# Kernel optimization log

Measured on AMD Instinct MI355X. Metric: run time of the kernel, lower is better.

The kernel has to match this reference:

```python
import jax, jax.numpy as jnp
import numpy as np

B, N, D, S, H, ITERS = 8, 2048, 256, 8, 256, 3
EPS = 1e-8
LN_EPS = 1e-5
SCALE = D ** -0.5


def _ln(x):
    # normalize over last axis (affine applied separately per slot)
    mu = jnp.mean(x, axis=-1, keepdims=True)
    var = jnp.var(x, axis=-1, keepdims=True)
    return (x - mu) / jnp.sqrt(var + LN_EPS)


def setup_inputs() -> dict:
    key = jax.random.key(0)
    ks = jax.random.split(key, 24)
    w = lambda k, shape, fan_in: jax.random.normal(k, shape, jnp.float32) / np.sqrt(fan_in)
    inp = {
        "inputs": jax.random.normal(ks[0], (B, N, D), jnp.float32),
        "slot_noise": jax.random.normal(ks[1], (B, S, D), jnp.float32),
        "slots_mu": jax.random.normal(ks[2], (1, S, D), jnp.float32),
        "slots_logsigma": 0.01 * jax.random.normal(ks[3], (1, S, D), jnp.float32),
        # per-slot LayerNorm affines [S, D]
        "g_in": jnp.ones((S, D), jnp.float32), "b_in": jnp.zeros((S, D), jnp.float32),
        "g_ns": jnp.ones((S, D), jnp.float32), "b_ns": jnp.zeros((S, D), jnp.float32),
        "g_pf": jnp.ones((S, D), jnp.float32), "b_pf": jnp.zeros((S, D), jnp.float32),
        # per-slot Linear weights [S, out, in] (torch convention)
        "Wq": w(ks[4], (S, D, D), D), "bq": jnp.zeros((S, D), jnp.float32),
        "Wk": w(ks[5], (S, D, D), D), "bk": jnp.zeros((S, D), jnp.float32),
        "Wv": w(ks[6], (S, D, D), D), "bv": jnp.zeros((S, D), jnp.float32),
        # per-slot GRUCell: [S, 3D, D] (gates order r, z, n as in torch)
        "W_ih": w(ks[7], (S, 3 * D, D), D), "b_ih": jnp.zeros((S, 3 * D), jnp.float32),
        "W_hh": w(ks[8], (S, 3 * D, D), D), "b_hh": jnp.zeros((S, 3 * D), jnp.float32),
        # per-slot MLP (dim -> hidden -> dim)
        "W1": w(ks[9], (S, H, D), D), "b1": jnp.zeros((S, H), jnp.float32),
        "W2": w(ks[10], (S, D, H), H), "b2": jnp.zeros((S, D), jnp.float32),
    }
    return inp


def slot_attention_fwd(inputs, slot_noise, slots_mu, slots_logsigma,
                       g_in, b_in, g_ns, b_ns, g_pf, b_pf,
                       Wq, bq, Wk, bk, Wv, bv,
                       W_ih, b_ih, W_hh, b_hh,
                       W1, b1, W2, b2):
    # slots init: mu + sigma * noise  -> [B, S, D]
    slots = slots_mu + jnp.exp(slots_logsigma) * slot_noise

    # per-slot LayerNorm of inputs: normalization is slot-independent, affine is per-slot
    xn = _ln(inputs)  # [B, N, D]
    inputs_n = xn[:, None, :, :] * g_in[None, :, None, :] + b_in[None, :, None, :]  # [B,S,N,D]

    # per-slot k/v projections as one batched GEMM over the slot axis
    k = jnp.einsum('bsnd,sod->bsno', inputs_n, Wk) + bk[None, :, None, :]  # [B,S,N,D]
    v = jnp.einsum('bsnd,sod->bsno', inputs_n, Wv) + bv[None, :, None, :]

    attn_ori = None
    for _ in range(ITERS):
        slots_prev = slots
        sn = _ln(slots) * g_ns[None] + b_ns[None]                     # [B,S,D]
        q = jnp.einsum('bsd,sod->bso', sn, Wq) + bq[None]             # [B,S,D]
        dots = jnp.einsum('bsd,bsnd->bsn', q, k) * SCALE              # [B,S,N]
        attn_ori = jax.nn.softmax(dots, axis=1) + EPS                 # softmax over slots
        attn = attn_ori / jnp.sum(attn_ori, axis=-1, keepdims=True)   # renormalize over n
        updates = jnp.einsum('bsnd,bsn->bsd', v, attn)                # [B,S,D]

        # per-slot GRUCell: h' = (1-z)*n + z*h
        gi = jnp.einsum('bsd,sod->bso', updates, W_ih) + b_ih[None]   # [B,S,3D]
        gh = jnp.einsum('bsd,sod->bso', slots_prev, W_hh) + b_hh[None]
        gi_r, gi_z, gi_n = jnp.split(gi, 3, axis=-1)
        gh_r, gh_z, gh_n = jnp.split(gh, 3, axis=-1)
        r = jax.nn.sigmoid(gi_r + gh_r)
        z = jax.nn.sigmoid(gi_z + gh_z)
        nn_ = jnp.tanh(gi_n + r * gh_n)
        slots = (1.0 - z) * nn_ + z * slots_prev

        # per-slot MLP residual
        pre = _ln(slots) * g_pf[None] + b_pf[None]
        h1 = jax.nn.relu(jnp.einsum('bsd,shd->bsh', pre, W1) + b1[None])
        slots = slots + jnp.einsum('bsh,sdh->bsd', h1, W2) + b2[None]

    return slots, attn_ori


def reference(inputs, slot_noise, slots_mu, slots_logsigma,
              g_in, b_in, g_ns, b_ns, g_pf, b_pf,
              Wq, bq, Wk, bk, Wv, bv,
              W_ih, b_ih, W_hh, b_hh,
              W1, b1, W2, b2):
    return slot_attention_fwd(inputs, slot_noise, slots_mu, slots_logsigma,
                              g_in, b_in, g_ns, b_ns, g_pf, b_pf,
                              Wq, bq, Wk, bk, Wv, bv,
                              W_ih, b_ih, W_hh, b_hh,
                              W1, b1, W2, b2)
```

## Files before the change

### kernel.cpp

```cpp
#include <hip/hip_runtime.h>


#define BB 8
#define NT 2048
#define DD 256
#define SS 8
#define HH 256

static constexpr float F_EPS   = 1e-8f;
static constexpr float F_LNEPS = 1e-5f;
static constexpr float F_SCALE = 0.0625f;

__device__ __forceinline__ float wredsum(float v) {
#pragma unroll
  for (int m = 32; m > 0; m >>= 1) v += __shfl_xor(v, m, 64);
  return v;
}
__device__ __forceinline__ float sigm(float x) { return 1.f / (1.f + __expf(-x)); }
__device__ __forceinline__ float tanhfast(float x) {
  float ax = fabsf(x);
  float e = __expf(2.f * ax);
  float t2 = 1.f - 2.f / (e + 1.f);
  return x < 0.f ? -t2 : t2;
}
__device__ __forceinline__ int x2i(int bb, int dd) { return bb*288 + (dd>>5)*36 + (dd&31); }
__device__ __forceinline__ int xpi(int d) { return (d>>5)*36 + (d&31); }

template <typename F>
__device__ __forceinline__ void gemv32(const float* __restrict__ Wrow0,
                                       const float* __restrict__ X2,
                                       float* __restrict__ part, F emit) {
  int t = threadIdx.x;
  int ol = t >> 3, dg = t & 7;
  const float4* wr = (const float4*)(Wrow0 + (size_t)ol*256 + (size_t)dg*32);
  __syncthreads();
  float acc[8] = {0.f,0.f,0.f,0.f,0.f,0.f,0.f,0.f};
#pragma unroll
  for (int j = 0; j < 8; ++j) {
    float4 w4 = wr[j];
    int xo = dg*36 + 4*j;
#pragma unroll
    for (int bbi = 0; bbi < 8; ++bbi) {
      float4 x4 = *(const float4*)&X2[bbi*288 + xo];
      acc[bbi] = fmaf(w4.x,x4.x, fmaf(w4.y,x4.y, fmaf(w4.z,x4.z, fmaf(w4.w,x4.w, acc[bbi]))));
    }
  }
#pragma unroll
  for (int bbi = 0; bbi < 8; ++bbi) part[(ol*8+bbi)*9 + dg] = acc[bbi];
  __syncthreads();
  int o = t >> 3, bbo = t & 7;
  const float* pp = &part[(o*8+bbo)*9];
  float v = ((pp[0]+pp[1])+(pp[2]+pp[3]))+((pp[4]+pp[5])+(pp[6]+pp[7]));
  emit(o, bbo, v);
}

template <typename F>
__device__ __forceinline__ void gemv32h(const float* __restrict__ Wrow0,
                                        const float* __restrict__ X2,
                                        float* __restrict__ part, int tid, F emit) {
  int ol = tid >> 3, dg = tid & 7;
  const float4* wr = (const float4*)(Wrow0 + (size_t)ol*256 + (size_t)dg*32);
  __syncthreads();
  float acc[8] = {0.f,0.f,0.f,0.f,0.f,0.f,0.f,0.f};
#pragma unroll
  for (int j = 0; j < 8; ++j) {
    float4 w4 = wr[j];
    int xo = dg*36 + 4*j;
#pragma unroll
    for (int bbi = 0; bbi < 8; ++bbi) {
      float4 x4 = *(const float4*)&X2[bbi*288 + xo];
      acc[bbi] = fmaf(w4.x,x4.x, fmaf(w4.y,x4.y, fmaf(w4.z,x4.z, fmaf(w4.w,x4.w, acc[bbi]))));
    }
  }
#pragma unroll
  for (int bbi = 0; bbi < 8; ++bbi) part[(ol*8+bbi)*9 + dg] = acc[bbi];
  __syncthreads();
  int o = tid >> 3, bbo = tid & 7;
  const float* pp = &part[(o*8+bbo)*9];
  float v = ((pp[0]+pp[1])+(pp[2]+pp[3]))+((pp[4]+pp[5])+(pp[6]+pp[7]));
  emit(o, bbo, v);
}

template <typename F>
__device__ __forceinline__ void gemv_tile(const float* __restrict__ Wrow0,
                                          const float* __restrict__ xp, F emit) {
  int t = threadIdx.x;
  int ol = t >> 3, dg = t & 7;
  const float4* wr = (const float4*)(Wrow0 + (size_t)ol*256 + dg*32);
  float acc = 0.f;
#pragma unroll
  for (int j = 0; j < 8; ++j) {
    float4 w4 = wr[j];
    float4 x4 = *(const float4*)&xp[dg*36 + 4*j];
    acc = fmaf(w4.x,x4.x, fmaf(w4.y,x4.y, fmaf(w4.z,x4.z, fmaf(w4.w,x4.w, acc))));
  }
  acc += __shfl_xor(acc, 1, 64);
  acc += __shfl_xor(acc, 2, 64);
  acc += __shfl_xor(acc, 4, 64);
  if ((t & 7) == 0) emit(ol, acc);
}

__global__ __launch_bounds__(256) void k_init(
    const float* __restrict__ Wk, const float* __restrict__ bk,
    const float* __restrict__ Wv, const float* __restrict__ bv,
    const float* __restrict__ b_in, const float* __restrict__ smu,
    const float* __restrict__ slsig, const float* __restrict__ noise,
    float* __restrict__ ck, float* __restrict__ cv, float* __restrict__ slots) {
  int blk = blockIdx.x;
  int t = threadIdx.x;
  if (blk < 32) {
    int s = blk >> 2, oq = blk & 3;
    int wid = t >> 6, lane = t & 63;
    float4 bi = ((const float4*)(b_in + s*DD))[lane];
    for (int r = 0; r < 16; ++r) {
      int o = oq*64 + wid*16 + r;
      float4 wk4 = ((const float4*)(Wk + ((size_t)s*DD + o)*DD))[lane];
      float4 wv4 = ((const float4*)(Wv + ((size_t)s*DD + o)*DD))[lane];
      float pk = wredsum(bi.x*wk4.x + bi.y*wk4.y + bi.z*wk4.z + bi.w*wk4.w);
      float pv = wredsum(bi.x*wv4.x + bi.y*wv4.y + bi.z*wv4.z + bi.w*wv4.w);
      if (lane == 0) {
        ck[s*DD+o] = pk + bk[s*DD+o];
        cv[s*DD+o] = pv + bv[s*DD+o];
      }
    }
  } else {
    int idx = (blk-32)*256 + t;
    int sd = idx & 2047;
    slots[idx] = smu[sd] + __expf(slsig[sd]) * noise[idx];
  }
}

__global__ __launch_bounds__(256) void k_init2(
    const float* __restrict__ Wq, const float* __restrict__ Wk,
    const float* __restrict__ bq, const float* __restrict__ ck,
    const float* __restrict__ g_in,
    float* __restrict__ Pg, float* __restrict__ vq,
    float* __restrict__ qcon, float* __restrict__ c0) {
  int blk = blockIdx.x;
  int t = threadIdx.x;
  if (blk < 512) {
    __shared__ float Ak[32*33], Aq[32*33];
    int s = blk >> 6, tile = blk & 63;
    int td = tile >> 3, te = tile & 7;
    int dl = t >> 5, el = t & 31;
    float acc[4] = {0.f,0.f,0.f,0.f};
    for (int o0 = 0; o0 < DD; o0 += 32) {
      __syncthreads();
      for (int i = t; i < 1024; i += 256) {
        int o = i >> 5, c = i & 31;
        Ak[o*33+c] = Wk[((size_t)s*DD + o0+o)*DD + td*32 + c];
        Aq[o*33+c] = Wq[((size_t)s*DD + o0+o)*DD + te*32 + c];
      }
      __syncthreads();
#pragma unroll 8
      for (int o = 0; o < 32; ++o) {
        float aq = Aq[o*33+el];
#pragma unroll
        for (int j = 0; j < 4; ++j)
          acc[j] += Ak[o*33 + dl*4 + j] * aq;
      }
    }
#pragma unroll
    for (int j = 0; j < 4; ++j) {
      int d = td*32 + dl*4 + j;
      Pg[((size_t)s*DD + d)*DD + te*32 + el] = g_in[s*DD + d] * acc[j];
    }
  } else {
    __shared__ float cvec[DD];
    __shared__ float part2[8*264];
    int idx = blk - 512;
    int s = idx >> 1, which = idx & 1;
    const float* W = which ? Wk : Wq;
    const float* vec = which ? bq : ck;
    cvec[t] = vec[s*DD + t];
    __syncthreads();
    int og = t >> 5, eg = t & 31;
    float acc[8] = {0.f,0.f,0.f,0.f,0.f,0.f,0.f,0.f};
    for (int oi = 0; oi < 32; ++oi) {
      int o = og*32 + oi;
      float cv2 = cvec[o];
      const float4* wrow = (const float4*)(W + ((size_t)s*DD + o)*DD + eg*8);
      float4 w0 = wrow[0], w1 = wrow[1];
      acc[0] += w0.x*cv2; acc[1] += w0.y*cv2; acc[2] += w0.z*cv2; acc[3] += w0.w*cv2;
      acc[4] += w1.x*cv2; acc[5] += w1.y*cv2; acc[6] += w1.z*cv2; acc[7] += w1.w*cv2;
    }
#pragma unroll
    for (int j = 0; j < 8; ++j) part2[og*264 + eg*8 + j] = acc[j];
    __syncthreads();
    float v = 0.f;
#pragma unroll
    for (int og2 = 0; og2 < 8; ++og2) v += part2[og2*264 + t];
    if (which) qcon[s*DD + t] = v * g_in[s*DD + t];
    else       vq[s*DD + t]   = v;
    if (which == 0 && t < 64) {
      float4 b4 = ((const float4*)(bq + s*DD))[t];
      float4 c4 = ((const float4*)(ck + s*DD))[t];
      float vv = wredsum(b4.x*c4.x + b4.y*c4.y + b4.z*c4.z + b4.w*c4.w);
      if (t == 0) c0[s] = vv;
    }
  }
}

__global__ __launch_bounds__(256) void k_init2b(
    const float* __restrict__ Wih, const float* __restrict__ Wv,
    const float* __restrict__ cv, const float* __restrict__ bih,
    float* __restrict__ Wiv, float* __restrict__ ci) {
  __shared__ float sm[2112];
  int blk = blockIdx.x;
  int t = threadIdx.x;
  if (blk < 1536) {
    float* Aih = sm;
    float* Bv  = sm + 1056;
    int s = blk / 192, rem = blk % 192;
    int tj = rem >> 3, td = rem & 7;
    int dl = t >> 5, el = t & 31;
    float acc[4] = {0.f,0.f,0.f,0.f};
    for (int o0 = 0; o0 < DD; o0 += 32) {
      __syncthreads();
      for (int i = t; i < 1024; i += 256) {
        int r = i >> 5, c = i & 31;
        Aih[r*33+c] = Wih[((size_t)s*768 + tj*32 + r)*DD + o0 + c];
        Bv[r*33+c]  = Wv[((size_t)s*DD + o0 + r)*DD + td*32 + c];
      }
      __syncthreads();
#pragma unroll 8
      for (int o = 0; o < 32; ++o) {
        float bv2 = Bv[o*33+el];
#pragma unroll
        for (int j = 0; j < 4; ++j)
          acc[j] += Aih[(dl*4+j)*33 + o] * bv2;
      }
    }
#pragma unroll
    for (int j = 0; j < 4; ++j) {
      int r = tj*32 + dl*4 + j;
      Wiv[((size_t)s*768 + r)*DD + td*32 + el] = acc[j];
    }
  } else {
    float* xp = sm;
    int idx = blk - 1536;
    int s = idx / 24, jt = idx % 24;
    xp[xpi(t)] = cv[s*DD + t];
    __syncthreads();
    gemv_tile(Wih + ((size_t)s*768 + jt*32)*DD, xp, [&](int o, float v){
      ci[s*768 + jt*32 + o] = v + bih[s*768 + jt*32 + o];
    });
  }
}

__global__ __launch_bounds__(256) void k_q2(
    const float* __restrict__ slots, const float* __restrict__ g_ns,
    const float* __restrict__ b_ns, const float* __restrict__ Pg,
    const float* __restrict__ qcon, const float* __restrict__ vq,
    const float* __restrict__ c0,
    float* __restrict__ qg, float* __restrict__ qc,
    float* __restrict__ axun, float* __restrict__ rsum) {
  __shared__ __align__(16) float X2[8*288];
  __shared__ float part[32*8*9];
  int blk = blockIdx.x;
  int s = blk >> 3, rc = blk & 7;
  int t = threadIdx.x;
  int wid = t >> 6, lane = t & 63;
  float4 g4 = ((const float4*)(g_ns + s*DD))[lane];
  float4 p4 = ((const float4*)(b_ns + s*DD))[lane];
#pragma unroll
  for (int half = 0; half < 2; ++half) {
    int bb2 = wid + half*4;
    const float4* src = (const float4*)(slots + (size_t)(bb2*8+s)*DD);
    float4 x = src[lane];
    float sv = wredsum(x.x+x.y+x.z+x.w);
    float sq = wredsum(x.x*x.x + x.y*x.y + x.z*x.z + x.w*x.w);
    float mu = sv*(1.f/DD), var = sq*(1.f/DD)-mu*mu, rs = rsqrtf(var+F_LNEPS);
    int base = bb2*288 + (lane>>3)*36 + (lane&7)*4;
    X2[base]   = (x.x-mu)*rs*g4.x + p4.x;
    X2[base+1] = (x.y-mu)*rs*g4.y + p4.y;
    X2[base+2] = (x.z-mu)*rs*g4.z + p4.z;
    X2[base+3] = (x.w-mu)*rs*g4.w + p4.w;
  }
  if (rc == 0) {
    for (int i = t; i < 2048; i += 256) {
      int bb2 = i >> 8, dd = i & 255;
      axun[(size_t)(bb2*8+s)*DD + dd] = 0.f;
    }
    if (t < 8) rsum[t*8+s] = 0.f;
  }
  __syncthreads();
  if (rc == 0) {
    int b = t >> 5, l32 = t & 31;
    float v = 0.f;
#pragma unroll
    for (int j = 0; j < 8; ++j)
      v += X2[b*288 + j*36 + l32] * vq[s*DD + j*32 + l32];
#pragma unroll
    for (int m = 16; m > 0; m >>= 1) v += __shfl_xor(v, m, 64);
    if (l32 == 0) qc[b*8+s] = v + c0[s];
  }
  gemv32(Pg + ((size_t)s*DD + rc*32)*DD, X2, part, [&](int o,int bb2,float v){
    qg[(size_t)(bb2*8+s)*DD + rc*32 + o] = v + qcon[s*DD + rc*32 + o];
  });
}

__global__ __launch_bounds__(256) void k_dots(
    const float* __restrict__ inputs, const float* __restrict__ qg,
    const float* __restrict__ qc, float* __restrict__ axun,
    float* __restrict__ rsum, float* __restrict__ attn_out, int write_attn) {
  __shared__ __align__(16) float qgl[SS*DD];
  __shared__ __align__(16) float xt[32*260];
  __shared__ float dl[8*33];
  __shared__ float qcl[8];
  __shared__ float rsl[8];
  int t = threadIdx.x;
  int b = blockIdx.x >> 5;
  int chunk = blockIdx.x & 31;
  int wid = t >> 6, lane = t & 63;
  for (int i = t; i < SS*DD; i += 256) qgl[i] = qg[(size_t)b*SS*DD + i];
  if (t < 8) { qcl[t] = qc[b*8+t]; rsl[t] = 0.f; }
  int si = t >> 5, ni = t & 31;
  float axa[8] = {0.f,0.f,0.f,0.f,0.f,0.f,0.f,0.f};
  for (int tile = 0; tile < 2; ++tile) {
    int n0 = (chunk*2 + tile) * 32;
    __syncthreads();
#pragma unroll
    for (int rr = 0; rr < 8; ++rr) {
      int r = wid*8 + rr;
      const float4* src = (const float4*)(inputs + ((size_t)b*NT + n0 + r)*DD);
      float4 x = src[lane];
      float sv = wredsum(x.x + x.y + x.z + x.w);
      float sq = wredsum(x.x*x.x + x.y*x.y + x.z*x.z + x.w*x.w);
      float mu = sv*(1.f/DD), var = sq*(1.f/DD)-mu*mu, rs = rsqrtf(var+F_LNEPS);
      float4 o;
      o.x=(x.x-mu)*rs; o.y=(x.y-mu)*rs; o.z=(x.z-mu)*rs; o.w=(x.w-mu)*rs;
      *(float4*)&xt[r*260 + lane*4] = o;
    }
    __syncthreads();
    float acc = 0.f;
    {
      const float4* xr = (const float4*)&xt[ni*260];
      const float4* qr = (const float4*)&qgl[si*DD];
#pragma unroll 8
      for (int j = 0; j < 64; ++j) {
        float4 a4 = xr[j]; float4 b4 = qr[j];
        acc += a4.x*b4.x + a4.y*b4.y + a4.z*b4.z + a4.w*b4.w;
      }
    }
    float dot = (acc + qcl[si]) * F_SCALE;
    dl[si*33+ni] = dot;
    __syncthreads();
    float m = dl[ni];
#pragma unroll
    for (int ss2 = 1; ss2 < 8; ++ss2) m = fmaxf(m, dl[ss2*33+ni]);
    float den = 0.f;
#pragma unroll
    for (int ss2 = 0; ss2 < 8; ++ss2) den += __expf(dl[ss2*33+ni] - m);
    float a = __expf(dot - m) / den + F_EPS;
    __syncthreads();
    dl[si*33+ni] = a;
    float rv = a;
#pragma unroll
    for (int mm = 16; mm > 0; mm >>= 1) rv += __shfl_xor(rv, mm, 64);
    if (ni == 0) rsl[si] += rv;
    if (write_attn) attn_out[(size_t)(b*8+si)*NT + n0 + ni] = a;
    __syncthreads();
#pragma unroll
    for (int n = 0; n < 32; ++n) {
      float x = xt[n*260 + t];
#pragma unroll
      for (int ss2 = 0; ss2 < 8; ++ss2) axa[ss2] += dl[ss2*33+n] * x;
    }
  }
#pragma unroll
  for (int ss2 = 0; ss2 < 8; ++ss2)
    atomicAdd(&axun[(size_t)(b*8+ss2)*DD + t], axa[ss2]);
  __syncthreads();
  if (t < 8) atomicAdd(&rsum[b*8+t], rsl[t]);
}

__global__ __launch_bounds__(512) void k_gru2(
    const float* __restrict__ slots, const float* __restrict__ axun,
    const float* __restrict__ rsum, const float* __restrict__ g_in,
    const float* __restrict__ Whh, const float* __restrict__ bhh,
    const float* __restrict__ Wiv, const float* __restrict__ ci,
    float* __restrict__ smid) {
  __shared__ __align__(16) float X2s[8*288];
  __shared__ __align__(16) float X2v[8*288];
  __shared__ float partA[32*8*9];
  __shared__ float partB[32*8*9];
  __shared__ float ghl[3*256];
  __shared__ float gil[3*256];
  int blk = blockIdx.x;
  int s = blk >> 3, jc = blk & 7, jb = jc*32;
  int t = threadIdx.x;
  int half = t >> 8, tid = t & 255;
  if (half == 0) {
    for (int i = tid; i < 2048; i += 256) {
      int b = i >> 8, d = i & 255;
      X2s[x2i(b,d)] = slots[(size_t)(b*8+s)*DD + d];
    }
  } else {
    for (int i = tid; i < 2048; i += 256) {
      int b = i >> 8, d = i & 255;
      X2v[x2i(b,d)] = axun[(size_t)(b*8+s)*DD + d] / rsum[b*8+s] * g_in[s*DD+d];
    }
  }
  for (int g = 0; g < 3; ++g) {
    const float* W = half ? (Wiv + ((size_t)s*768 + g*256 + jb)*DD)
                          : (Whh + ((size_t)s*768 + g*256 + jb)*DD);
    const float* X = half ? X2v : X2s;
    float* pt = half ? partB : partA;
    float* out = half ? gil : ghl;
    const float* bias = half ? ci : bhh;
    gemv32h(W, X, pt, tid, [&](int o,int b,float v){
      out[g*256 + o*8 + b] = v + bias[s*768 + g*256 + jb + o];
    });
  }
  __syncthreads();
  if (half == 0) {
    int o = tid >> 3, b = tid & 7;
    int d = jb + o;
    float hprev = X2s[x2i(b,d)];
    float r = sigm(gil[o*8+b] + ghl[o*8+b]);
    float z = sigm(gil[256 + o*8+b] + ghl[256 + o*8+b]);
    float nn2 = tanhfast(gil[512 + o*8+b] + r*ghl[512 + o*8+b]);
    smid[(size_t)(b*8+s)*DD + d] = (1.f - z)*nn2 + z*hprev;
  }
}

__global__ __launch_bounds__(256) void k_mlp1(
    const float* __restrict__ smid, const float* __restrict__ g_pf,
    const float* __restrict__ b_pf, const float* __restrict__ W1,
    const float* __restrict__ b1, float* __restrict__ h1b) {
  __shared__ __align__(16) float X2[8*288];
  __shared__ float part[32*8*9];
  int blk = blockIdx.x;
  int s = blk >> 3, rc = blk & 7;
  int t = threadIdx.x;
  int wid = t >> 6, lane = t & 63;
#pragma unroll
  for (int half = 0; half < 2; ++half) {
    int bb2 = wid + half*4;
    const float4* src = (const float4*)(smid + (size_t)(bb2*8+s)*DD);
    float4 x = src[lane];
    float sv = wredsum(x.x+x.y+x.z+x.w);
    float sq = wredsum(x.x*x.x + x.y*x.y + x.z*x.z + x.w*x.w);
    float mu = sv*(1.f/DD), var = sq*(1.f/DD)-mu*mu, rs = rsqrtf(var+F_LNEPS);
    float4 g4 = ((const float4*)(g_pf + s*DD))[lane];
    float4 p4 = ((const float4*)(b_pf + s*DD))[lane];
    int base = bb2*288 + (lane>>3)*36 + (lane&7)*4;
    X2[base]   = (x.x-mu)*rs*g4.x + p4.x;
    X2[base+1] = (x.y-mu)*rs*g4.y + p4.y;
    X2[base+2] = (x.z-mu)*rs*g4.z + p4.z;
    X2[base+3] = (x.w-mu)*rs*g4.w + p4.w;
  }
  gemv32(W1 + ((size_t)s*HH + rc*32)*DD, X2, part, [&](int o,int bb2,float v){
    float rr = v + b1[s*HH + rc*32 + o];
    h1b[(size_t)(bb2*8+s)*HH + rc*32 + o] = fmaxf(rr, 0.f);
  });
}

__global__ __launch_bounds__(256) void k_mlp2(
    const float* __restrict__ h1b, const float* __restrict__ W2,
    const float* __restrict__ b2, const float* __restrict__ smid,
    float* __restrict__ slots, float* __restrict__ out_slots, int last) {
  __shared__ __align__(16) float X2[8*288];
  __shared__ float part[32*8*9];
  int blk = blockIdx.x;
  int s = blk >> 3, rc = blk & 7;
  int t = threadIdx.x;
  for (int i = t; i < 2048; i += 256) {
    int bb2 = i >> 8, dd = i & 255;
    X2[x2i(bb2,dd)] = h1b[(size_t)(bb2*8+s)*HH + dd];
  }
  gemv32(W2 + ((size_t)s*DD + rc*32)*HH, X2, part, [&](int o,int bb2,float v){
    int d = rc*32 + o;
    size_t idx = (size_t)(bb2*8+s)*DD + d;
    float rr = v + b2[s*DD + d] + smid[idx];
    slots[idx] = rr;
    if (last) out_slots[idx] = rr;
  });
}

extern "C" void kernel_launch(void* const* d_in, const int* in_sizes, int n_in,
                              void* d_out, int out_size, void* d_ws, size_t ws_size,
                              hipStream_t stream) {
  (void)in_sizes; (void)n_in; (void)out_size; (void)ws_size;
  const float* inputs = (const float*)d_in[0];
  const float* noise  = (const float*)d_in[1];
  const float* smu    = (const float*)d_in[2];
  const float* slsig  = (const float*)d_in[3];
  const float* g_in   = (const float*)d_in[4];
  const float* b_in   = (const float*)d_in[5];
  const float* g_ns   = (const float*)d_in[6];
  const float* b_ns   = (const float*)d_in[7];
  const float* g_pf   = (const float*)d_in[8];
  const float* b_pf   = (const float*)d_in[9];
  const float* Wq  = (const float*)d_in[10];
  const float* bq  = (const float*)d_in[11];
  const float* Wk  = (const float*)d_in[12];
  const float* bk  = (const float*)d_in[13];
  const float* Wv  = (const float*)d_in[14];
  const float* bv  = (const float*)d_in[15];
  const float* Wih = (const float*)d_in[16];
  const float* bih = (const float*)d_in[17];
  const float* Whh = (const float*)d_in[18];
  const float* bhh = (const float*)d_in[19];
  const float* W1  = (const float*)d_in[20];
  const float* b1  = (const float*)d_in[21];
  const float* W2  = (const float*)d_in[22];
  const float* b2  = (const float*)d_in[23];

  float* ws = (float*)d_ws;
  float* slots  = ws;                 ws += BB*SS*DD;
  float* smid   = ws;                 ws += BB*SS*DD;
  float* ck     = ws;                 ws += SS*DD;
  float* cv     = ws;                 ws += SS*DD;
  float* qg     = ws;                 ws += BB*SS*DD;
  float* qc     = ws;                 ws += 64;
  float* rsum   = ws;                 ws += 64;
  float* axun   = ws;                 ws += BB*SS*DD;
  float* h1b    = ws;                 ws += BB*SS*HH;
  float* vq     = ws;                 ws += SS*DD;
  float* qcon   = ws;                 ws += SS*DD;
  float* c0     = ws;                 ws += 64;
  float* ci     = ws;                 ws += SS*768;
  float* Pg     = ws;                 ws += (size_t)SS*DD*DD;
  float* Wiv    = ws;                 ws += (size_t)SS*768*DD;

  float* out_slots = (float*)d_out;
  float* out_attn  = out_slots + BB*SS*DD;

  k_init<<<dim3(96), dim3(256), 0, stream>>>(Wk, bk, Wv, bv, b_in, smu, slsig, noise,
                                             ck, cv, slots);
  k_init2<<<dim3(528), dim3(256), 0, stream>>>(Wq, Wk, bq, ck, g_in, Pg, vq, qcon, c0);
  k_init2b<<<dim3(1728), dim3(256), 0, stream>>>(Wih, Wv, cv, bih, Wiv, ci);
  k_q2<<<dim3(64), dim3(256), 0, stream>>>(slots, g_ns, b_ns, Pg, qcon, vq, c0,
                                           qg, qc, axun, rsum);
  for (int it = 0; it < 3; ++it) {
    int last = (it == 2) ? 1 : 0;
    k_dots<<<dim3(256), dim3(256), 0, stream>>>(inputs, qg, qc, axun, rsum,
                                                out_attn, last);
    k_gru2<<<dim3(64), dim3(512), 0, stream>>>(slots, axun, rsum, g_in,
                                               Whh, bhh, Wiv, ci, smid);
    k_mlp1<<<dim3(64), dim3(256), 0, stream>>>(smid, g_pf, b_pf, W1, b1, h1b);
    k_mlp2<<<dim3(64), dim3(256), 0, stream>>>(h1b, W2, b2, smid, slots,
                                               out_slots, last);
    if (!last)
      k_q2<<<dim3(64), dim3(256), 0, stream>>>(slots, g_ns, b_ns, Pg, qcon, vq, c0,
                                               qg, qc, axun, rsum);
  }
}
```

Measured before the change: 215.7 us.

## Merge weight-precompute GEMMs into one kernel with 64x64 register-tiled blocks

```diff
diff --git a/kernel.cpp b/kernel.cpp
--- a/kernel.cpp
+++ b/kernel.cpp
@@ -100,16 +100,87 @@
   if ((t & 7) == 0) emit(ol, acc);
 }
 
-__global__ __launch_bounds__(256) void k_init(
-    const float* __restrict__ Wk, const float* __restrict__ bk,
-    const float* __restrict__ Wv, const float* __restrict__ bv,
+__global__ __launch_bounds__(256) void k_setup1(
+    const float* __restrict__ Wq, const float* __restrict__ Wk,
+    const float* __restrict__ Wv, const float* __restrict__ Wih,
+    const float* __restrict__ bk, const float* __restrict__ bv,
     const float* __restrict__ b_in, const float* __restrict__ smu,
     const float* __restrict__ slsig, const float* __restrict__ noise,
-    float* __restrict__ ck, float* __restrict__ cv, float* __restrict__ slots) {
+    const float* __restrict__ g_in,
+    float* __restrict__ Pg, float* __restrict__ Wiv,
+    float* __restrict__ ck, float* __restrict__ cv,
+    float* __restrict__ slots) {
   int blk = blockIdx.x;
   int t = threadIdx.x;
-  if (blk < 32) {
-    int s = blk >> 2, oq = blk & 3;
+  if (blk < 512) {
+    __shared__ __align__(16) float As[32*68];
+    __shared__ __align__(16) float Bs[32*68];
+    bool isPg = blk < 128;
+    int s, d0, e0;
+    if (isPg) { s = blk >> 4; int tl2 = blk & 15; d0 = (tl2>>2)*64; e0 = (tl2&3)*64; }
+    else { int b2 = blk-128; s = b2/48; int rem = b2%48; d0 = (rem>>2)*64; e0 = (rem&3)*64; }
+    int ty = t >> 4, tx = t & 15;
+    float acc[4][4] = {{0.f,0.f,0.f,0.f},{0.f,0.f,0.f,0.f},{0.f,0.f,0.f,0.f},{0.f,0.f,0.f,0.f}};
+    const float* Abase = isPg ? (Wk + (size_t)s*DD*DD) : (Wih + (size_t)s*768*DD);
+    const float* Bbase = isPg ? (Wq + (size_t)s*DD*DD) : (Wv + (size_t)s*DD*DD);
+    for (int o0 = 0; o0 < DD; o0 += 32) {
+      __syncthreads();
+      if (isPg) {
+        for (int l = t; l < 512; l += 256) {
+          int o = l >> 4, dq = l & 15;
+          *(float4*)&As[o*68 + dq*4] = *(const float4*)&Abase[(size_t)(o0+o)*DD + d0 + dq*4];
+        }
+      } else {
+        for (int l = t; l < 512; l += 256) {
+          int r = l >> 3, oq = l & 7;
+          float4 v = *(const float4*)&Abase[(size_t)(d0+r)*DD + o0 + oq*4];
+          As[(oq*4+0)*68 + r] = v.x;
+          As[(oq*4+1)*68 + r] = v.y;
+          As[(oq*4+2)*68 + r] = v.z;
+          As[(oq*4+3)*68 + r] = v.w;
+        }
+      }
+      for (int l = t; l < 512; l += 256) {
+        int o = l >> 4, eq = l & 15;
+        *(float4*)&Bs[o*68 + eq*4] = *(const float4*)&Bbase[(size_t)(o0+o)*DD + e0 + eq*4];
+      }
+      __syncthreads();
+#pragma unroll 8
+      for (int o = 0; o < 32; ++o) {
+        float4 a4 = *(const float4*)&As[o*68 + ty*4];
+        float4 b4 = *(const float4*)&Bs[o*68 + tx*4];
+        float av[4] = {a4.x,a4.y,a4.z,a4.w};
+        float bw[4] = {b4.x,b4.y,b4.z,b4.w};
+#pragma unroll
+        for (int i = 0; i < 4; ++i)
+#pragma unroll
+          for (int j = 0; j < 4; ++j)
+            acc[i][j] = fmaf(av[i], bw[j], acc[i][j]);
+      }
+    }
+    if (isPg) {
+#pragma unroll
+      for (int i = 0; i < 4; ++i) {
+        int d = d0 + ty*4 + i;
+        float g = g_in[s*DD + d];
+        float4 o4 = {g*acc[i][0], g*acc[i][1], g*acc[i][2], g*acc[i][3]};
+        *(float4*)&Pg[((size_t)s*DD + d)*DD + e0 + tx*4] = o4;
+      }
+    } else {
+#pragma unroll
+      for (int i = 0; i < 4; ++i) {
+        int r = d0 + ty*4 + i;
+        float4 o4 = {acc[i][0], acc[i][1], acc[i][2], acc[i][3]};
+        *(float4*)&Wiv[((size_t)s*768 + r)*DD + e0 + tx*4] = o4;
+      }
+    }
+  } else if (blk < 576) {
+    int idx = (blk-512)*256 + t;
+    int sd = idx & 2047;
+    slots[idx] = smu[sd] + __expf(slsig[sd]) * noise[idx];
+  } else {
+    int bb = blk - 576;
+    int s = bb >> 2, oq = bb & 3;
     int wid = t >> 6, lane = t & 63;
     float4 bi = ((const float4*)(b_in + s*DD))[lane];
     for (int r = 0; r < 16; ++r) {
@@ -123,53 +194,23 @@
         cv[s*DD+o] = pv + bv[s*DD+o];
       }
     }
-  } else {
-    int idx = (blk-32)*256 + t;
-    int sd = idx & 2047;
-    slots[idx] = smu[sd] + __expf(slsig[sd]) * noise[idx];
-  }
-}
-
-__global__ __launch_bounds__(256) void k_init2(
+  }
+}
+
+__global__ __launch_bounds__(256) void k_setup2(
     const float* __restrict__ Wq, const float* __restrict__ Wk,
-    const float* __restrict__ bq, const float* __restrict__ ck,
-    const float* __restrict__ g_in,
-    float* __restrict__ Pg, float* __restrict__ vq,
-    float* __restrict__ qcon, float* __restrict__ c0) {
+    const float* __restrict__ Wih, const float* __restrict__ bq,
+    const float* __restrict__ bih, const float* __restrict__ ck,
+    const float* __restrict__ cv, const float* __restrict__ g_in,
+    float* __restrict__ vq, float* __restrict__ qcon,
+    float* __restrict__ c0, float* __restrict__ ci) {
+  __shared__ __align__(16) float sm[8*264];
   int blk = blockIdx.x;
   int t = threadIdx.x;
-  if (blk < 512) {
-    __shared__ float Ak[32*33], Aq[32*33];
-    int s = blk >> 6, tile = blk & 63;
-    int td = tile >> 3, te = tile & 7;
-    int dl = t >> 5, el = t & 31;
-    float acc[4] = {0.f,0.f,0.f,0.f};
-    for (int o0 = 0; o0 < DD; o0 += 32) {
-      __syncthreads();
-      for (int i = t; i < 1024; i += 256) {
-        int o = i >> 5, c = i & 31;
-        Ak[o*33+c] = Wk[((size_t)s*DD + o0+o)*DD + td*32 + c];
-        Aq[o*33+c] = Wq[((size_t)s*DD + o0+o)*DD + te*32 + c];
-      }
-      __syncthreads();
-#pragma unroll 8
-      for (int o = 0; o < 32; ++o) {
-        float aq = Aq[o*33+el];
-#pragma unroll
-        for (int j = 0; j < 4; ++j)
-          acc[j] += Ak[o*33 + dl*4 + j] * aq;
-      }
-    }
-#pragma unroll
-    for (int j = 0; j < 4; ++j) {
-      int d = td*32 + dl*4 + j;
-      Pg[((size_t)s*DD + d)*DD + te*32 + el] = g_in[s*DD + d] * acc[j];
-    }
-  } else {
-    __shared__ float cvec[DD];
+  if (blk < 16) {
+    float* cvec  = sm;
     __shared__ float part2[8*264];
-    int idx = blk - 512;
-    int s = idx >> 1, which = idx & 1;
+    int s = blk >> 1, which = blk & 1;
     const float* W = which ? Wk : Wq;
     const float* vec = which ? bq : ck;
     cvec[t] = vec[s*DD + t];
@@ -178,11 +219,11 @@
     float acc[8] = {0.f,0.f,0.f,0.f,0.f,0.f,0.f,0.f};
     for (int oi = 0; oi < 32; ++oi) {
       int o = og*32 + oi;
-      float cv2 = cvec[o];
+      float cw = cvec[o];
       const float4* wrow = (const float4*)(W + ((size_t)s*DD + o)*DD + eg*8);
       float4 w0 = wrow[0], w1 = wrow[1];
-      acc[0] += w0.x*cv2; acc[1] += w0.y*cv2; acc[2] += w0.z*cv2; acc[3] += w0.w*cv2;
-      acc[4] += w1.x*cv2; acc[5] += w1.y*cv2; acc[6] += w1.z*cv2; acc[7] += w1.w*cv2;
+      acc[0] += w0.x*cw; acc[1] += w0.y*cw; acc[2] += w0.z*cw; acc[3] += w0.w*cw;
+      acc[4] += w1.x*cw; acc[5] += w1.y*cw; acc[6] += w1.z*cw; acc[7] += w1.w*cw;
     }
 #pragma unroll
     for (int j = 0; j < 8; ++j) part2[og*264 + eg*8 + j] = acc[j];
@@ -198,47 +239,9 @@
       float vv = wredsum(b4.x*c4.x + b4.y*c4.y + b4.z*c4.z + b4.w*c4.w);
       if (t == 0) c0[s] = vv;
     }
-  }
-}
-
-__global__ __launch_bounds__(256) void k_init2b(
-    const float* __restrict__ Wih, const float* __restrict__ Wv,
-    const float* __restrict__ cv, const float* __restrict__ bih,
-    float* __restrict__ Wiv, float* __restrict__ ci) {
-  __shared__ float sm[2112];
-  int blk = blockIdx.x;
-  int t = threadIdx.x;
-  if (blk < 1536) {
-    float* Aih = sm;
-    float* Bv  = sm + 1056;
-    int s = blk / 192, rem = blk % 192;
-    int tj = rem >> 3, td = rem & 7;
-    int dl = t >> 5, el = t & 31;
-    float acc[4] = {0.f,0.f,0.f,0.f};
-    for (int o0 = 0; o0 < DD; o0 += 32) {
-      __syncthreads();
-      for (int i = t; i < 1024; i += 256) {
-        int r = i >> 5, c = i & 31;
-        Aih[r*33+c] = Wih[((size_t)s*768 + tj*32 + r)*DD + o0 + c];
-        Bv[r*33+c]  = Wv[((size_t)s*DD + o0 + r)*DD + td*32 + c];
-      }
-      __syncthreads();
-#pragma unroll 8
-      for (int o = 0; o < 32; ++o) {
-        float bv2 = Bv[o*33+el];
-#pragma unroll
-        for (int j = 0; j < 4; ++j)
-          acc[j] += Aih[(dl*4+j)*33 + o] * bv2;
-      }
-    }
-#pragma unroll
-    for (int j = 0; j < 4; ++j) {
-      int r = tj*32 + dl*4 + j;
-      Wiv[((size_t)s*768 + r)*DD + td*32 + el] = acc[j];
-    }
   } else {
     float* xp = sm;
-    int idx = blk - 1536;
+    int idx = blk - 16;
     int s = idx / 24, jt = idx % 24;
     xp[xpi(t)] = cv[s*DD + t];
     __syncthreads();
@@ -528,10 +531,11 @@
   float* out_slots = (float*)d_out;
   float* out_attn  = out_slots + BB*SS*DD;
 
-  k_init<<<dim3(96), dim3(256), 0, stream>>>(Wk, bk, Wv, bv, b_in, smu, slsig, noise,
-                                             ck, cv, slots);
-  k_init2<<<dim3(528), dim3(256), 0, stream>>>(Wq, Wk, bq, ck, g_in, Pg, vq, qcon, c0);
-  k_init2b<<<dim3(1728), dim3(256), 0, stream>>>(Wih, Wv, cv, bih, Wiv, ci);
+  k_setup1<<<dim3(608), dim3(256), 0, stream>>>(Wq, Wk, Wv, Wih, bk, bv, b_in,
+                                                smu, slsig, noise, g_in,
+                                                Pg, Wiv, ck, cv, slots);
+  k_setup2<<<dim3(208), dim3(256), 0, stream>>>(Wq, Wk, Wih, bq, bih, ck, cv, g_in,
+                                                vq, qcon, c0, ci);
   k_q2<<<dim3(64), dim3(256), 0, stream>>>(slots, g_ns, b_ns, Pg, qcon, vq, c0,
                                            qg, qc, axun, rsum);
   for (int it = 0; it < 3; ++it) {
```

Result: faster. 182.0 us (-15.6%).
